# Performance work log

Measured on AMD Instinct MI355X. Metric: run time of the kernel, lower is better.

## Reference

```python
import jax, jax.numpy as jnp
import numpy as np

D = 1024
B = 128
N = 576
MAX_LEN = 5000
TEMP = 1.0


def build_pe(max_len, d):
    position = jnp.arange(max_len, dtype=jnp.float32)[:, None]
    div_term = jnp.exp(jnp.arange(0, d, 2, dtype=jnp.float32) * (-np.log(10000.0) / d))
    pe = jnp.zeros((max_len, d), dtype=jnp.float32)
    pe = pe.at[:, 0::2].set(jnp.sin(position * div_term))
    pe = pe.at[:, 1::2].set(jnp.cos(position * div_term))
    return pe  # [max_len, d]


def setup_inputs() -> dict:
    key = jax.random.key(0)
    ks = jax.random.split(key, 16)
    s = 0.02
    inp = {
        "x": jax.random.normal(ks[0], (B, N), dtype=jnp.float32),
        "timesteps": jax.random.randint(ks[1], (B,), 0, 1000),
        "text_feat": jax.random.normal(ks[2], (B, D), dtype=jnp.float32),
        "image_feat": jax.random.normal(ks[3], (B, N, D), dtype=jnp.float32),
        # projections (torch Linear stored as [in, out] here; bias=False for q/k/v)
        "Wq": jax.random.normal(ks[4], (D, D), dtype=jnp.float32) * s,
        "Wk": jax.random.normal(ks[5], (D, D), dtype=jnp.float32) * s,
        "Wv": jax.random.normal(ks[6], (D, D), dtype=jnp.float32) * s,
        "Wp": jax.random.normal(ks[7], (D, D), dtype=jnp.float32) * s,
        "bp": jnp.zeros((D,), dtype=jnp.float32),
        # timestep embedder MLP
        "Wt1": jax.random.normal(ks[8], (D, D), dtype=jnp.float32) * s,
        "bt1": jnp.zeros((D,), dtype=jnp.float32),
        "Wt2": jax.random.normal(ks[9], (D, D), dtype=jnp.float32) * s,
        "bt2": jnp.zeros((D,), dtype=jnp.float32),
        # decoder MLP: 2d -> 2d -> 1
        "Wd1": jax.random.normal(ks[10], (2 * D, 2 * D), dtype=jnp.float32) * s,
        "bd1": jnp.zeros((2 * D,), dtype=jnp.float32),
        "Wd2": jax.random.normal(ks[11], (2 * D, 1), dtype=jnp.float32) * s,
        "bd2": jnp.zeros((1,), dtype=jnp.float32),
    }
    return inp


def reference(x, timesteps, text_feat, image_feat, Wq, Wk, Wv, Wp, bp,
              Wt1, bt1, Wt2, bt2, Wd1, bd1, Wd2, bd2):
    pe = build_pe(MAX_LEN, D)
    # timestep conditioning: MLP(pe[t])  -> [B, d]
    t_emb = pe[timesteps]                                   # [B, d]
    cond = jax.nn.silu(t_emb @ Wt1 + bt1) @ Wt2 + bt2       # [B, d]

    # image re-weighting by text similarity
    i_w = jax.nn.softmax(jnp.einsum('bd,bnd->bn', text_feat, image_feat) / TEMP, axis=-1)
    img = image_feat * i_w[:, :, None]                      # [B, n, d]

    q = (text_feat + cond) @ Wq                             # [B, d]
    k = (img + cond[:, None, :]) @ Wk                       # [B, n, d]
    v = (img + cond[:, None, :]) @ Wv                       # [B, n, d]

    weight = jax.nn.softmax(jnp.einsum('bd,bnd->bn', q, k) + x, axis=-1)  # [B, n]
    new_emb = jnp.einsum('bn,bnd->bd', weight, v) @ Wp + bp               # [B, d]

    # decoder on concat([new_emb broadcast, img])  -> [B, n, 2d] -> [B, n]
    emb = jnp.concatenate([jnp.broadcast_to(new_emb[:, None, :], img.shape), img], axis=-1)
    h = jax.nn.relu(emb @ Wd1 + bd1)
    p = (h @ Wd2 + bd2)[..., 0]                             # [B, n]
    return p + weight
```

## Files before the change

kernel.cpp:

```cpp
#include <hip/hip_runtime.h>
#include <hip/hip_bf16.h>
#include <cmath>

#define D_    1024
#define B_    128
#define N_    576
#define ROWS_ (B_*N_)
#define TWOD_ 2048
#define TAU_  1e-5f
#define NU_   8

__device__ __forceinline__ float waveReduceSum(float v){
  #pragma unroll
  for (int m=32;m;m>>=1) v += __shfl_xor(v,m,64);
  return v;
}
__device__ __forceinline__ float waveReduceMax(float v){
  #pragma unroll
  for (int m=32;m;m>>=1) v = fmaxf(v,__shfl_xor(v,m,64));
  return v;
}

__global__ __launch_bounds__(256) void k_init(float* wimg, float* p_corr, int* count){
  int i = blockIdx.x*256 + threadIdx.x;
  if (i < B_*D_) wimg[i] = 0.f;
  if (i < ROWS_) p_corr[i] = 0.f;
  if (i == 0) *count = 0;
}

__global__ __launch_bounds__(256) void k_temb(const int* __restrict__ ts, float* __restrict__ temb){
  int b = blockIdx.x;
  float t = (float)ts[b];
  for (int i=threadIdx.x; i<D_/2; i+=256){
    float dv = expf((float)(2*i) * (-9.210340371976184f/(float)D_));
    float a = t*dv;
    temb[b*D_ + 2*i]   = sinf(a);
    temb[b*D_ + 2*i+1] = cosf(a);
  }
}

__global__ __launch_bounds__(256) void k_gemm(const float* __restrict__ A, const float* __restrict__ W,
    int ldw, const float* __restrict__ bias, float* __restrict__ C, int nout, int act, int tmode){
  __shared__ float a0[D_], a1[D_];
  int r0 = blockIdx.y*2;
  for (int i=threadIdx.x;i<D_;i+=256){ a0[i]=A[r0*D_+i]; a1[i]=A[(r0+1)*D_+i]; }
  __syncthreads();
  int col = blockIdx.x*256 + threadIdx.x;
  float acc0=0.f, acc1=0.f;
  if (tmode==0){
    const float* wp = W + col;
    #pragma unroll 8
    for (int k=0;k<D_;k++){
      float wv = wp[(size_t)k*ldw];
      acc0 = fmaf(a0[k],wv,acc0);
      acc1 = fmaf(a1[k],wv,acc1);
    }
  } else {
    const float* wp = W + (size_t)col*ldw;
    #pragma unroll 8
    for (int k=0;k<D_;k++){
      float wv = wp[k];
      acc0 = fmaf(a0[k],wv,acc0);
      acc1 = fmaf(a1[k],wv,acc1);
    }
  }
  float bb = bias ? bias[col] : 0.f;
  float o0=acc0+bb, o1=acc1+bb;
  if (act==1){ o0 = o0/(1.f+expf(-o0)); o1 = o1/(1.f+expf(-o1)); }
  C[(size_t)r0*nout+col]=o0; C[(size_t)(r0+1)*nout+col]=o1;
}

__global__ __launch_bounds__(256) void k_dots(const float* __restrict__ text,
    const float* __restrict__ imgf, float* __restrict__ s){
  int wave = threadIdx.x>>6, lane = threadIdx.x&63;
  int row = blockIdx.x*4 + wave;
  int b = row / N_;
  const float4* ip = (const float4*)(imgf + (size_t)row*D_);
  const float4* tp = (const float4*)(text + (size_t)b*D_);
  float acc=0.f;
  #pragma unroll
  for (int p=0;p<4;p++){
    float4 a = ip[p*64+lane];
    float4 t = tp[p*64+lane];
    acc = fmaf(a.x,t.x,acc); acc = fmaf(a.y,t.y,acc);
    acc = fmaf(a.z,t.z,acc); acc = fmaf(a.w,t.w,acc);
  }
  acc = waveReduceSum(acc);
  if (lane==0) s[row]=acc;
}

__global__ __launch_bounds__(256) void k_softmax(const float* __restrict__ s, float* __restrict__ w,
    int buildList, int* count, int* lrow, float* liw){
  int b = blockIdx.x;
  __shared__ float rbuf[4];
  const float* sp = s + b*N_;
  float m = -3e38f;
  for (int i=threadIdx.x;i<N_;i+=256) m = fmaxf(m, sp[i]);
  m = waveReduceMax(m);
  if ((threadIdx.x&63)==0) rbuf[threadIdx.x>>6]=m;
  __syncthreads();
  m = fmaxf(fmaxf(rbuf[0],rbuf[1]),fmaxf(rbuf[2],rbuf[3]));
  __syncthreads();
  float sum=0.f;
  for (int i=threadIdx.x;i<N_;i+=256) sum += expf(sp[i]-m);
  sum = waveReduceSum(sum);
  if ((threadIdx.x&63)==0) rbuf[threadIdx.x>>6]=sum;
  __syncthreads();
  sum = rbuf[0]+rbuf[1]+rbuf[2]+rbuf[3];
  float inv = 1.f/sum;
  float* wp = w + b*N_;
  for (int i=threadIdx.x;i<N_;i+=256){
    float wi = expf(sp[i]-m)*inv;
    wp[i]=wi;
    if (buildList && wi > TAU_){
      int pos = atomicAdd(count,1);
      if (pos < ROWS_){ lrow[pos]=b*N_+i; liw[pos]=wi; }
    }
  }
}

__global__ __launch_bounds__(256) void k_lbase(const float* __restrict__ x, float* __restrict__ s){
  int i = blockIdx.x*256+threadIdx.x;
  if (i<ROWS_) s[i]=x[i];
}

__global__ __launch_bounds__(256) void k_lsparse(const float* __restrict__ x, const float* __restrict__ imgf,
    const float* __restrict__ kq, const int* __restrict__ count, const int* __restrict__ lrow,
    const float* __restrict__ liw, float* __restrict__ s){
  int wave=threadIdx.x>>6, lane=threadIdx.x&63;
  int cnt = min(*count, ROWS_);
  for (int e = blockIdx.x*4+wave; e<cnt; e += gridDim.x*4){
    int row=lrow[e], b=row/N_; float iw=liw[e];
    const float4* ip=(const float4*)(imgf+(size_t)row*D_);
    const float4* kp=(const float4*)(kq + b*D_);
    float acc=0.f;
    #pragma unroll
    for (int p=0;p<4;p++){
      int c = p*64+lane;
      float4 a = ip[c];
      float4 k = kp[c];
      acc = fmaf(a.x,k.x,acc); acc = fmaf(a.y,k.y,acc);
      acc = fmaf(a.z,k.z,acc); acc = fmaf(a.w,k.w,acc);
    }
    acc = waveReduceSum(acc);
    if (lane==0) s[row] = x[row] + iw*acc;
  }
}

__global__ __launch_bounds__(256) void k_wimg(const float* __restrict__ imgf, const float* __restrict__ wgt,
    const int* __restrict__ count, const int* __restrict__ lrow,
    const float* __restrict__ liw, float* __restrict__ wimg){
  int cnt = min(*count, ROWS_);
  for (int e = blockIdx.x; e<cnt; e += gridDim.x){
    int row=lrow[e], b=row/N_;
    float coef = liw[e]*wgt[row];
    const float* src = imgf + (size_t)row*D_;
    for (int i=threadIdx.x;i<D_;i+=256)
      atomicAdd(&wimg[b*D_+i], coef*src[i]);
  }
}

__global__ __launch_bounds__(256) void k_addff(const float* __restrict__ a, const float* __restrict__ b,
    float* __restrict__ o){
  int i = blockIdx.x*256+threadIdx.x;
  if (i<B_*D_) o[i]=a[i]+b[i];
}

__global__ __launch_bounds__(256) void k_p0(const float* __restrict__ r, const float* __restrict__ wd2,
    const float* __restrict__ bd2, float* __restrict__ p0){
  __shared__ float rbuf[4];
  int b=blockIdx.x;
  float acc=0.f;
  for (int j=threadIdx.x;j<TWOD_;j+=256)
    acc = fmaf(fmaxf(r[b*TWOD_+j],0.f), wd2[j], acc);
  acc = waveReduceSum(acc);
  if((threadIdx.x&63)==0) rbuf[threadIdx.x>>6]=acc;
  __syncthreads();
  if (threadIdx.x==0) p0[b] = rbuf[0]+rbuf[1]+rbuf[2]+rbuf[3] + bd2[0];
}

__global__ __launch_bounds__(256) void k_corr(const float* __restrict__ imgf, const float* __restrict__ Wd1,
    const float* __restrict__ r, const float* __restrict__ wd2, const int* __restrict__ count,
    const int* __restrict__ lrow, const float* __restrict__ liw,
    float* __restrict__ p_corr){
  __shared__ __align__(16) float img[D_][NU_];
  __shared__ float rbuf[4];
  int j = blockIdx.x*256 + threadIdx.x;
  float wd2j = wd2[j];
  int cnt = min(*count, ROWS_);
  int NG = gridDim.y;
  for (int base = blockIdx.y*NU_; base < cnt; base += NG*NU_){
    int nu = min(NU_, cnt-base);
    __syncthreads();
    for (int u=0;u<nu;u++){
      const float* src = imgf + (size_t)lrow[base+u]*D_;
      for (int i=threadIdx.x;i<D_;i+=256) img[i][u]=src[i];
    }
    for (int u=nu;u<NU_;u++)
      for (int i=threadIdx.x;i<D_;i+=256) img[i][u]=0.f;
    __syncthreads();
    float g[NU_];
    #pragma unroll
    for (int u=0;u<NU_;u++) g[u]=0.f;
    const float* wp = Wd1 + (size_t)D_*TWOD_ + j;
    #pragma unroll 4
    for (int e=0;e<D_;e++){
      float wv = wp[(size_t)e*TWOD_];
      const float4* ir = (const float4*)(&img[e][0]);
      float4 i0 = ir[0], i1 = ir[1];
      g[0]=fmaf(i0.x,wv,g[0]); g[1]=fmaf(i0.y,wv,g[1]);
      g[2]=fmaf(i0.z,wv,g[2]); g[3]=fmaf(i0.w,wv,g[3]);
      g[4]=fmaf(i1.x,wv,g[4]); g[5]=fmaf(i1.y,wv,g[5]);
      g[6]=fmaf(i1.z,wv,g[6]); g[7]=fmaf(i1.w,wv,g[7]);
    }
    for (int u=0;u<nu;u++){
      int row = lrow[base+u];
      float rv = r[(size_t)(row/N_)*TWOD_ + j];
      float c  = rv + liw[base+u]*g[u];
      float contrib = (fmaxf(c,0.f)-fmaxf(rv,0.f))*wd2j;
      contrib = waveReduceSum(contrib);
      if ((threadIdx.x&63)==0) rbuf[threadIdx.x>>6]=contrib;
      __syncthreads();
      if (threadIdx.x==0) atomicAdd(&p_corr[row], rbuf[0]+rbuf[1]+rbuf[2]+rbuf[3]);
      __syncthreads();
    }
  }
}

__global__ __launch_bounds__(256) void k_final(const float* __restrict__ p0, const float* __restrict__ p_corr,
    const float* __restrict__ wgt, float* __restrict__ out){
  int i = blockIdx.x*256+threadIdx.x;
  if (i<ROWS_){
    int b = i/N_;
    out[i] = p0[b] + p_corr[i] + wgt[i];
  }
}

extern "C" void kernel_launch(void* const* d_in, const int* in_sizes, int n_in,
                              void* d_out, int out_size, void* d_ws, size_t ws_size,
                              hipStream_t stream) {
  const float* x    = (const float*)d_in[0];
  const int*   ts   = (const int*)  d_in[1];
  const float* text = (const float*)d_in[2];
  const float* imgf = (const float*)d_in[3];
  const float* Wq   = (const float*)d_in[4];
  const float* Wk   = (const float*)d_in[5];
  const float* Wv   = (const float*)d_in[6];
  const float* Wp   = (const float*)d_in[7];
  const float* bp   = (const float*)d_in[8];
  const float* Wt1  = (const float*)d_in[9];
  const float* bt1  = (const float*)d_in[10];
  const float* Wt2  = (const float*)d_in[11];
  const float* bt2  = (const float*)d_in[12];
  const float* Wd1  = (const float*)d_in[13];
  const float* bd1  = (const float*)d_in[14];
  const float* Wd2  = (const float*)d_in[15];
  const float* bd2  = (const float*)d_in[16];
  float* out = (float*)d_out;

  float* f = (float*)d_ws;
  float* bufA  = f;
  float* bufB  = f +  131072;
  float* cond  = f +  262144;
  float* wimg  = f +  393216;
  float* rbuf  = f +  524288;
  float* sbuf  = f +  786432;
  float* wgt   = f +  860160;
  float* pcorr = f +  933888;
  float* liw   = f + 1007616;
  int*   lrow  = (int*)(f + 1081344);
  float* p0    = f + 1155072;
  int*   cnt   = (int*)(f + 1155200);

  k_init<<<512,256,0,stream>>>(wimg, pcorr, cnt);
  k_temb<<<B_,256,0,stream>>>(ts, bufA);
  k_gemm<<<dim3(4,64),256,0,stream>>>(bufA, Wt1, D_, bt1, bufB, D_, 1, 0);
  k_gemm<<<dim3(4,64),256,0,stream>>>(bufB, Wt2, D_, bt2, cond, D_, 0, 0);
  k_dots<<<ROWS_/4,256,0,stream>>>(text, imgf, sbuf);
  k_softmax<<<B_,256,0,stream>>>(sbuf, sbuf, 1, cnt, lrow, liw);
  k_addff<<<512,256,0,stream>>>(text, cond, bufA);
  k_gemm<<<dim3(4,64),256,0,stream>>>(bufA, Wq, D_, nullptr, bufB, D_, 0, 0);
  k_gemm<<<dim3(4,64),256,0,stream>>>(bufB, Wk, D_, nullptr, bufA, D_, 0, 1);
  k_lbase<<<(ROWS_+255)/256,256,0,stream>>>(x, sbuf);
  k_lsparse<<<64,256,0,stream>>>(x, imgf, bufA, cnt, lrow, liw, sbuf);
  k_softmax<<<B_,256,0,stream>>>(sbuf, wgt, 0, cnt, lrow, liw);
  k_wimg<<<128,256,0,stream>>>(imgf, wgt, cnt, lrow, liw, wimg);
  k_addff<<<512,256,0,stream>>>(wimg, cond, bufB);
  k_gemm<<<dim3(4,64),256,0,stream>>>(bufB, Wv, D_, nullptr, bufA, D_, 0, 0);
  k_gemm<<<dim3(4,64),256,0,stream>>>(bufA, Wp, D_, bp, bufB, D_, 0, 0);
  k_gemm<<<dim3(8,64),256,0,stream>>>(bufB, Wd1, TWOD_, bd1, rbuf, TWOD_, 0, 0);
  k_p0<<<B_,256,0,stream>>>(rbuf, Wd2, bd2, p0);
  k_corr<<<dim3(8,64),256,0,stream>>>(imgf, Wd1, rbuf, Wd2, cnt, lrow, liw, pcorr);
  k_final<<<(ROWS_+255)/256,256,0,stream>>>(p0, pcorr, wgt, out);
}
```

Baseline: 1.054 ms.

## Split-K the small GEMMs with atomics and fuse init, bias, activation and adds

Replaces the 2-row GEMM with a split-K (4-way) 4-row GEMM that accumulates into output with atomicAdd. Bias, SiLU and residual adds are folded into the init and GEMM prologue kernels, and the temb, lbase and addff launches are merged or removed. This raises parallelism for the batch-128 GEMMs and improves weight reuse per load, and it cuts the number of launches. In exchange, float atomics make the results nondeterministic, and a large init pass now writes all accumulators. The unroll of the k_corr loop also rises to 8.

```diff
diff --git a/kernel.cpp b/kernel.cpp
--- a/kernel.cpp
+++ b/kernel.cpp
@@ -21,53 +21,78 @@
   return v;
 }
 
-__global__ __launch_bounds__(256) void k_init(float* wimg, float* p_corr, int* count){
-  int i = blockIdx.x*256 + threadIdx.x;
-  if (i < B_*D_) wimg[i] = 0.f;
-  if (i < ROWS_) p_corr[i] = 0.f;
-  if (i == 0) *count = 0;
-}
-
-__global__ __launch_bounds__(256) void k_temb(const int* __restrict__ ts, float* __restrict__ temb){
-  int b = blockIdx.x;
-  float t = (float)ts[b];
-  for (int i=threadIdx.x; i<D_/2; i+=256){
-    float dv = expf((float)(2*i) * (-9.210340371976184f/(float)D_));
-    float a = t*dv;
-    temb[b*D_ + 2*i]   = sinf(a);
-    temb[b*D_ + 2*i+1] = cosf(a);
-  }
-}
-
-__global__ __launch_bounds__(256) void k_gemm(const float* __restrict__ A, const float* __restrict__ W,
-    int ldw, const float* __restrict__ bias, float* __restrict__ C, int nout, int act, int tmode){
-  __shared__ float a0[D_], a1[D_];
-  int r0 = blockIdx.y*2;
-  for (int i=threadIdx.x;i<D_;i+=256){ a0[i]=A[r0*D_+i]; a1[i]=A[(r0+1)*D_+i]; }
+__global__ __launch_bounds__(256) void k_init0(const int* __restrict__ ts,
+    float* __restrict__ temb, float* __restrict__ h1, float* __restrict__ cond,
+    float* __restrict__ qv, float* __restrict__ kq, float* __restrict__ wv,
+    float* __restrict__ newemb, float* __restrict__ rbuf, float* __restrict__ wimg,
+    float* __restrict__ pcorr, float* __restrict__ sdelta, int* __restrict__ cnt,
+    const float* __restrict__ bt1, const float* __restrict__ bt2,
+    const float* __restrict__ bp, const float* __restrict__ bd1){
+  int bid = blockIdx.x;
+  if (bid < 128){
+    float t = (float)ts[bid];
+    for (int i=threadIdx.x; i<512; i+=256){
+      float dv = expf((float)(2*i) * (-9.210340371976184f/1024.f));
+      float a = t*dv;
+      temb[bid*D_ + 2*i]   = sinf(a);
+      temb[bid*D_ + 2*i+1] = cosf(a);
+    }
+    return;
+  }
+  int idx0 = (bid-128)*256 + threadIdx.x;
+  int stride = (gridDim.x-128)*256;
+  if (idx0 == 0) *cnt = 0;
+  for (int j=idx0; j<1327104; j+=stride){
+    if      (j <  131072) h1[j]            = bt1[j&1023];
+    else if (j <  262144) cond[j-131072]   = bt2[j&1023];
+    else if (j <  393216) qv[j-262144]     = 0.f;
+    else if (j <  524288) kq[j-393216]     = 0.f;
+    else if (j <  655360) wv[j-524288]     = 0.f;
+    else if (j <  786432) newemb[j-655360] = bp[j&1023];
+    else if (j < 1048576) rbuf[j-786432]   = bd1[(j-786432)&2047];
+    else if (j < 1179648) wimg[j-1048576]  = 0.f;
+    else if (j < 1253376) pcorr[j-1179648] = 0.f;
+    else                  sdelta[j-1253376]= 0.f;
+  }
+}
+
+__global__ __launch_bounds__(256) void k_gemm2(const float* __restrict__ A,
+    const float* __restrict__ A2, const float* __restrict__ W, int ldw,
+    float* __restrict__ C, int nout, int mode, int tmode){
+  __shared__ float a[4][256];
+  int r0 = blockIdx.y*4;
+  int kbase = blockIdx.z*256;
+  #pragma unroll
+  for (int r=0;r<4;r++){
+    float v = A[(size_t)(r0+r)*D_ + kbase + threadIdx.x];
+    if (mode==1) v = v/(1.f+expf(-v));
+    else if (mode==2) v += A2[(size_t)(r0+r)*D_ + kbase + threadIdx.x];
+    a[r][threadIdx.x] = v;
+  }
   __syncthreads();
   int col = blockIdx.x*256 + threadIdx.x;
-  float acc0=0.f, acc1=0.f;
+  float acc0=0.f, acc1=0.f, acc2=0.f, acc3=0.f;
   if (tmode==0){
-    const float* wp = W + col;
+    const float* wp = W + (size_t)kbase*ldw + col;
     #pragma unroll 8
-    for (int k=0;k<D_;k++){
+    for (int k=0;k<256;k++){
       float wv = wp[(size_t)k*ldw];
-      acc0 = fmaf(a0[k],wv,acc0);
-      acc1 = fmaf(a1[k],wv,acc1);
+      acc0=fmaf(a[0][k],wv,acc0); acc1=fmaf(a[1][k],wv,acc1);
+      acc2=fmaf(a[2][k],wv,acc2); acc3=fmaf(a[3][k],wv,acc3);
     }
   } else {
-    const float* wp = W + (size_t)col*ldw;
+    const float* wp = W + (size_t)col*ldw + kbase;
     #pragma unroll 8
-    for (int k=0;k<D_;k++){
+    for (int k=0;k<256;k++){
       float wv = wp[k];
-      acc0 = fmaf(a0[k],wv,acc0);
-      acc1 = fmaf(a1[k],wv,acc1);
-    }
-  }
-  float bb = bias ? bias[col] : 0.f;
-  float o0=acc0+bb, o1=acc1+bb;
-  if (act==1){ o0 = o0/(1.f+expf(-o0)); o1 = o1/(1.f+expf(-o1)); }
-  C[(size_t)r0*nout+col]=o0; C[(size_t)(r0+1)*nout+col]=o1;
+      acc0=fmaf(a[0][k],wv,acc0); acc1=fmaf(a[1][k],wv,acc1);
+      acc2=fmaf(a[2][k],wv,acc2); acc3=fmaf(a[3][k],wv,acc3);
+    }
+  }
+  atomicAdd(&C[(size_t)(r0  )*nout+col], acc0);
+  atomicAdd(&C[(size_t)(r0+1)*nout+col], acc1);
+  atomicAdd(&C[(size_t)(r0+2)*nout+col], acc2);
+  atomicAdd(&C[(size_t)(r0+3)*nout+col], acc3);
 }
 
 __global__ __launch_bounds__(256) void k_dots(const float* __restrict__ text,
@@ -89,8 +114,8 @@
   if (lane==0) s[row]=acc;
 }
 
-__global__ __launch_bounds__(256) void k_softmax(const float* __restrict__ s, float* __restrict__ w,
-    int buildList, int* count, int* lrow, float* liw){
+__global__ __launch_bounds__(256) void k_softmax1(const float* __restrict__ s,
+    int* count, int* lrow, float* liw){
   int b = blockIdx.x;
   __shared__ float rbuf[4];
   const float* sp = s + b*N_;
@@ -108,25 +133,18 @@
   __syncthreads();
   sum = rbuf[0]+rbuf[1]+rbuf[2]+rbuf[3];
   float inv = 1.f/sum;
-  float* wp = w + b*N_;
   for (int i=threadIdx.x;i<N_;i+=256){
     float wi = expf(sp[i]-m)*inv;
-    wp[i]=wi;
-    if (buildList && wi > TAU_){
+    if (wi > TAU_){
       int pos = atomicAdd(count,1);
       if (pos < ROWS_){ lrow[pos]=b*N_+i; liw[pos]=wi; }
     }
   }
 }
 
-__global__ __launch_bounds__(256) void k_lbase(const float* __restrict__ x, float* __restrict__ s){
-  int i = blockIdx.x*256+threadIdx.x;
-  if (i<ROWS_) s[i]=x[i];
-}
-
-__global__ __launch_bounds__(256) void k_lsparse(const float* __restrict__ x, const float* __restrict__ imgf,
+__global__ __launch_bounds__(256) void k_lsparse(const float* __restrict__ imgf,
     const float* __restrict__ kq, const int* __restrict__ count, const int* __restrict__ lrow,
-    const float* __restrict__ liw, float* __restrict__ s){
+    const float* __restrict__ liw, float* __restrict__ sdelta){
   int wave=threadIdx.x>>6, lane=threadIdx.x&63;
   int cnt = min(*count, ROWS_);
   for (int e = blockIdx.x*4+wave; e<cnt; e += gridDim.x*4){
@@ -143,12 +161,37 @@
       acc = fmaf(a.z,k.z,acc); acc = fmaf(a.w,k.w,acc);
     }
     acc = waveReduceSum(acc);
-    if (lane==0) s[row] = x[row] + iw*acc;
-  }
-}
-
-__global__ __launch_bounds__(256) void k_wimg(const float* __restrict__ imgf, const float* __restrict__ wgt,
-    const int* __restrict__ count, const int* __restrict__ lrow,
+    if (lane==0) sdelta[row] = iw*acc;
+  }
+}
+
+__global__ __launch_bounds__(256) void k_softmax2(const float* __restrict__ x,
+    const float* __restrict__ sdelta, float* __restrict__ w){
+  int b = blockIdx.x;
+  __shared__ float rbuf[4];
+  const float* xp = x + b*N_;
+  const float* dp = sdelta + b*N_;
+  float m = -3e38f;
+  for (int i=threadIdx.x;i<N_;i+=256) m = fmaxf(m, xp[i]+dp[i]);
+  m = waveReduceMax(m);
+  if ((threadIdx.x&63)==0) rbuf[threadIdx.x>>6]=m;
+  __syncthreads();
+  m = fmaxf(fmaxf(rbuf[0],rbuf[1]),fmaxf(rbuf[2],rbuf[3]));
+  __syncthreads();
+  float sum=0.f;
+  for (int i=threadIdx.x;i<N_;i+=256) sum += expf(xp[i]+dp[i]-m);
+  sum = waveReduceSum(sum);
+  if ((threadIdx.x&63)==0) rbuf[threadIdx.x>>6]=sum;
+  __syncthreads();
+  sum = rbuf[0]+rbuf[1]+rbuf[2]+rbuf[3];
+  float inv = 1.f/sum;
+  float* wp = w + b*N_;
+  for (int i=threadIdx.x;i<N_;i+=256)
+    wp[i] = expf(xp[i]+dp[i]-m)*inv;
+}
+
+__global__ __launch_bounds__(256) void k_wimg(const float* __restrict__ imgf,
+    const float* __restrict__ wgt, const int* __restrict__ count, const int* __restrict__ lrow,
     const float* __restrict__ liw, float* __restrict__ wimg){
   int cnt = min(*count, ROWS_);
   for (int e = blockIdx.x; e<cnt; e += gridDim.x){
@@ -160,14 +203,8 @@
   }
 }
 
-__global__ __launch_bounds__(256) void k_addff(const float* __restrict__ a, const float* __restrict__ b,
-    float* __restrict__ o){
-  int i = blockIdx.x*256+threadIdx.x;
-  if (i<B_*D_) o[i]=a[i]+b[i];
-}
-
-__global__ __launch_bounds__(256) void k_p0(const float* __restrict__ r, const float* __restrict__ wd2,
-    const float* __restrict__ bd2, float* __restrict__ p0){
+__global__ __launch_bounds__(256) void k_p0(const float* __restrict__ r,
+    const float* __restrict__ wd2, const float* __restrict__ bd2, float* __restrict__ p0){
   __shared__ float rbuf[4];
   int b=blockIdx.x;
   float acc=0.f;
@@ -179,9 +216,9 @@
   if (threadIdx.x==0) p0[b] = rbuf[0]+rbuf[1]+rbuf[2]+rbuf[3] + bd2[0];
 }
 
-__global__ __launch_bounds__(256) void k_corr(const float* __restrict__ imgf, const float* __restrict__ Wd1,
-    const float* __restrict__ r, const float* __restrict__ wd2, const int* __restrict__ count,
-    const int* __restrict__ lrow, const float* __restrict__ liw,
+__global__ __launch_bounds__(256) void k_corr(const float* __restrict__ imgf,
+    const float* __restrict__ Wd1, const float* __restrict__ r, const float* __restrict__ wd2,
+    const int* __restrict__ count, const int* __restrict__ lrow, const float* __restrict__ liw,
     float* __restrict__ p_corr){
   __shared__ __align__(16) float img[D_][NU_];
   __shared__ float rbuf[4];
@@ -203,7 +240,7 @@
     #pragma unroll
     for (int u=0;u<NU_;u++) g[u]=0.f;
     const float* wp = Wd1 + (size_t)D_*TWOD_ + j;
-    #pragma unroll 4
+    #pragma unroll 8
     for (int e=0;e<D_;e++){
       float wv = wp[(size_t)e*TWOD_];
       const float4* ir = (const float4*)(&img[e][0]);
@@ -227,8 +264,8 @@
   }
 }
 
-__global__ __launch_bounds__(256) void k_final(const float* __restrict__ p0, const float* __restrict__ p_corr,
-    const float* __restrict__ wgt, float* __restrict__ out){
+__global__ __launch_bounds__(256) void k_final(const float* __restrict__ p0,
+    const float* __restrict__ p_corr, const float* __restrict__ wgt, float* __restrict__ out){
   int i = blockIdx.x*256+threadIdx.x;
   if (i<ROWS_){
     int b = i/N_;
@@ -259,36 +296,38 @@
   float* out = (float*)d_out;
 
   float* f = (float*)d_ws;
-  float* bufA  = f;
-  float* bufB  = f +  131072;
-  float* cond  = f +  262144;
-  float* wimg  = f +  393216;
-  float* rbuf  = f +  524288;
-  float* sbuf  = f +  786432;
-  float* wgt   = f +  860160;
-  float* pcorr = f +  933888;
-  float* liw   = f + 1007616;
-  int*   lrow  = (int*)(f + 1081344);
-  float* p0    = f + 1155072;
-  int*   cnt   = (int*)(f + 1155200);
-
-  k_init<<<512,256,0,stream>>>(wimg, pcorr, cnt);
-  k_temb<<<B_,256,0,stream>>>(ts, bufA);
-  k_gemm<<<dim3(4,64),256,0,stream>>>(bufA, Wt1, D_, bt1, bufB, D_, 1, 0);
-  k_gemm<<<dim3(4,64),256,0,stream>>>(bufB, Wt2, D_, bt2, cond, D_, 0, 0);
+  float* temb   = f;
+  float* h1     = f +  131072;
+  float* cond   = f +  262144;
+  float* qv     = f +  393216;
+  float* kq     = f +  524288;
+  float* wv     = f +  655360;
+  float* newemb = f +  786432;
+  float* rbuf   = f +  917504;
+  float* wimg   = f + 1179648;
+  float* sbuf   = f + 1310720;
+  float* wgt    = f + 1384448;
+  float* pcorr  = f + 1458176;
+  float* sdelta = f + 1531904;
+  float* liw    = f + 1605632;
+  int*   lrow   = (int*)(f + 1679360);
+  float* p0     = f + 1753088;
+  int*   cnt    = (int*)(f + 1753216);
+
+  k_init0<<<1152,256,0,stream>>>(ts, temb, h1, cond, qv, kq, wv, newemb, rbuf,
+                                 wimg, pcorr, sdelta, cnt, bt1, bt2, bp, bd1);
+  k_gemm2<<<dim3(4,32,4),256,0,stream>>>(temb, nullptr, Wt1, D_, h1,   D_, 0, 0);
+  k_gemm2<<<dim3(4,32,4),256,0,stream>>>(h1,   nullptr, Wt2, D_, cond, D_, 1, 0);
   k_dots<<<ROWS_/4,256,0,stream>>>(text, imgf, sbuf);
-  k_softmax<<<B_,256,0,stream>>>(sbuf, sbuf, 1, cnt, lrow, liw);
-  k_addff<<<512,256,0,stream>>>(text, cond, bufA);
-  k_gemm<<<dim3(4,64),256,0,stream>>>(bufA, Wq, D_, nullptr, bufB, D_, 0, 0);
-  k_gemm<<<dim3(4,64),256,0,stream>>>(bufB, Wk, D_, nullptr, bufA, D_, 0, 1);
-  k_lbase<<<(ROWS_+255)/256,256,0,stream>>>(x, sbuf);
-  k_lsparse<<<64,256,0,stream>>>(x, imgf, bufA, cnt, lrow, liw, sbuf);
-  k_softmax<<<B_,256,0,stream>>>(sbuf, wgt, 0, cnt, lrow, liw);
+  k_softmax1<<<B_,256,0,stream>>>(sbuf, cnt, lrow, liw);
+  k_gemm2<<<dim3(4,32,4),256,0,stream>>>(text, cond, Wq, D_, qv, D_, 2, 0);
+  k_gemm2<<<dim3(4,32,4),256,0,stream>>>(qv, nullptr, Wk, D_, kq, D_, 0, 1);
+  k_lsparse<<<64,256,0,stream>>>(imgf, kq, cnt, lrow, liw, sdelta);
+  k_softmax2<<<B_,256,0,stream>>>(x, sdelta, wgt);
   k_wimg<<<128,256,0,stream>>>(imgf, wgt, cnt, lrow, liw, wimg);
-  k_addff<<<512,256,0,stream>>>(wimg, cond, bufB);
-  k_gemm<<<dim3(4,64),256,0,stream>>>(bufB, Wv, D_, nullptr, bufA, D_, 0, 0);
-  k_gemm<<<dim3(4,64),256,0,stream>>>(bufA, Wp, D_, bp, bufB, D_, 0, 0);
-  k_gemm<<<dim3(8,64),256,0,stream>>>(bufB, Wd1, TWOD_, bd1, rbuf, TWOD_, 0, 0);
+  k_gemm2<<<dim3(4,32,4),256,0,stream>>>(wimg, cond, Wv, D_, wv, D_, 2, 0);
+  k_gemm2<<<dim3(4,32,4),256,0,stream>>>(wv, nullptr, Wp, D_, newemb, D_, 0, 0);
+  k_gemm2<<<dim3(8,32,4),256,0,stream>>>(newemb, nullptr, Wd1, TWOD_, rbuf, TWOD_, 0, 0);
   k_p0<<<B_,256,0,stream>>>(rbuf, Wd2, bd2, p0);
   k_corr<<<dim3(8,64),256,0,stream>>>(imgf, Wd1, rbuf, Wd2, cnt, lrow, liw, pcorr);
   k_final<<<(ROWS_+255)/256,256,0,stream>>>(p0, pcorr, wgt, out);
```

Measured after the change: 1.120 ms. 6.2% more time.
